# Kernel tuning notes

Hardware: AMD Instinct MI355X
Metric: run time of the kernel (lower is better)

The kernel has to match this reference:

```python
import jax, jax.numpy as jnp
import numpy as np
import math

B, S, H, NH, DH, FF = 8, 512, 1024, 16, 64, 4096


def _layer_norm(x, gamma, beta, eps=1e-12):
    m = jnp.mean(x, axis=-1, keepdims=True)
    v = jnp.mean(jnp.square(x - m), axis=-1, keepdims=True)
    return (x - m) * jax.lax.rsqrt(v + eps) * gamma + beta


def setup_inputs() -> dict:
    key = jax.random.key(0)
    ks = jax.random.split(key, 12)
    w = lambda k, shape: jax.random.normal(k, shape, jnp.float32) * 0.02
    return {
        "layer_input": jax.random.normal(ks[0], (B * S, H), jnp.float32),
        "attention_mask": jax.random.randint(ks[1], (B, S, S), 0, 2, jnp.int32),
        "Wq": w(ks[2], (H, H)), "bq": jnp.zeros((H,), jnp.float32),
        "Wk": w(ks[3], (H, H)), "bk": jnp.zeros((H,), jnp.float32),
        "Wv": w(ks[4], (H, H)), "bv": jnp.zeros((H,), jnp.float32),
        "Wao": w(ks[5], (H, H)), "bao": jnp.zeros((H,), jnp.float32),
        "gamma1": jnp.ones((H,), jnp.float32), "beta1": jnp.zeros((H,), jnp.float32),
        "Wi": w(ks[6], (H, FF)), "bi": jnp.zeros((FF,), jnp.float32),
        "Wo": w(ks[7], (FF, H)), "bo": jnp.zeros((H,), jnp.float32),
        "gamma2": jnp.ones((H,), jnp.float32), "beta2": jnp.zeros((H,), jnp.float32),
        "batch_size": B,
        "seq_length": S,
    }


def reference(layer_input, attention_mask, Wq, bq, Wk, bk, Wv, bv, Wao, bao,
              gamma1, beta1, Wi, bi, Wo, bo, gamma2, beta2, batch_size, seq_length):
    Bs, Sl = batch_size, seq_length
    # QKV projections on flattened [B*S, H]
    q = layer_input @ Wq + bq
    k = layer_input @ Wk + bk
    v = layer_input @ Wv + bv
    # [B*S, H] -> [B, NH, S, DH]
    split = lambda t: t.reshape(Bs, Sl, NH, DH).transpose(0, 2, 1, 3)
    qh, kh, vh = split(q), split(k), split(v)
    # scaled dot-product scores [B, NH, S, S]
    scores = jnp.einsum("bhqd,bhkd->bhqk", qh, kh) * (1.0 / math.sqrt(DH))
    adder = (1.0 - attention_mask[:, None].astype(jnp.float32)) * -10000.0
    probs = jax.nn.softmax(scores + adder, axis=-1)
    # context [B, NH, S, DH] -> [B*S, H]
    ctx = jnp.einsum("bhqk,bhkd->bhqd", probs, vh)
    ctx = ctx.transpose(0, 2, 1, 3).reshape(Bs * Sl, NH * DH)
    attn_out = _layer_norm(ctx @ Wao + bao + layer_input, gamma1, beta1)
    inter = jax.nn.gelu(attn_out @ Wi + bi, approximate=True)  # BERT tanh-gelu
    out = _layer_norm(inter @ Wo + bo + attn_out, gamma2, beta2)
    return out
```

## Files before the change

kernel.cpp:

```cpp
#include <hip/hip_runtime.h>
#include <stdint.h>
#include <math.h>

typedef __attribute__((ext_vector_type(8))) short bf16x8;
typedef __attribute__((ext_vector_type(4))) float f32x4;
typedef __attribute__((ext_vector_type(4))) unsigned short us4;

#define BB   8
#define SS   512
#define HH   1024
#define NHH  16
#define DHH  64
#define FFF  4096
#define MTOK 4096
#define QKVN 3072

__device__ __forceinline__ unsigned short f2bf(float f) {
  union { float f; uint32_t u; } c; c.f = f;
  uint32_t u = c.u;
  return (unsigned short)((u + 0x7fffu + ((u >> 16) & 1u)) >> 16);
}

__device__ __forceinline__ float gelu_tanh(float x) {
  float u = 0.7978845608028654f * (x + 0.044715f * x * x * x);
  return x / (1.0f + __expf(-2.0f * u));
}

__device__ __forceinline__ void gload16(const unsigned short* g, unsigned short* l) {
  __builtin_amdgcn_global_load_lds(
      (const __attribute__((address_space(1))) unsigned short*)g,
      (__attribute__((address_space(3))) unsigned short*)l, 16, 0, 0);
}

__global__ void cast_f32_to_bf16(const float* __restrict__ in,
                                 unsigned short* __restrict__ out, int n4) {
  int i = blockIdx.x * blockDim.x + threadIdx.x;
  if (i >= n4) return;
  f32x4 v = *(const f32x4*)(in + (size_t)i * 4);
  us4 o;
  #pragma unroll
  for (int j = 0; j < 4; ++j) o[j] = f2bf(v[j]);
  *(us4*)(out + (size_t)i * 4) = o;
}

__global__ void transpose_cast(const float* __restrict__ in,
                               unsigned short* __restrict__ out, int R, int C) {
  __shared__ float tile[32][33];
  int bc = blockIdx.x * 32, br = blockIdx.y * 32;
  int tx = threadIdx.x, ty = threadIdx.y;
  #pragma unroll
  for (int i = 0; i < 32; i += 8)
    tile[ty + i][tx] = in[(size_t)(br + ty + i) * C + bc + tx];
  __syncthreads();
  #pragma unroll
  for (int i = 0; i < 32; i += 8)
    out[(size_t)(bc + ty + i) * R + br + tx] = f2bf(tile[tx][ty + i]);
}

__global__ void concat3(const float* __restrict__ a, const float* __restrict__ b,
                        const float* __restrict__ c, float* __restrict__ o) {
  int i = blockIdx.x * 256 + threadIdx.x;
  o[i] = i < HH ? a[i] : (i < 2 * HH ? b[i - HH] : c[i - 2 * HH]);
}

template <int EPI>
__global__ __launch_bounds__(512, 2) void gemm8(
    const unsigned short* __restrict__ A, const unsigned short* __restrict__ BT,
    const float* __restrict__ bias, unsigned short* __restrict__ Cb,
    float* __restrict__ Cf, int M, int N, int K, int KSL) {
  __shared__ unsigned short Asl[2][256 * 64];
  __shared__ unsigned short Bsl[2][256 * 64];
  const int t = threadIdx.x;
  const int w = t >> 6, lane = t & 63;
  const int g = lane >> 4, fr = lane & 15;
  const int wr = w >> 2, wc = w & 3;
  const int m0 = blockIdx.x * 256, n0 = blockIdx.y * 256;
  const int k0 = blockIdx.z * KSL;
  const int nk = KSL >> 6;

  const int srow = t >> 3;
  const int schunk = (t & 7) ^ (srow & 7);
  const unsigned short* gA = A + (size_t)(m0 + srow) * K + k0 + schunk * 8;
  const unsigned short* gB = BT + (size_t)(n0 + srow) * K + k0 + schunk * 8;

  f32x4 acc[8][4] = {};

  #define STAGE(buf, kt)                                                 \
    _Pragma("unroll")                                                    \
    for (int j = 0; j < 4; ++j) {                                        \
      gload16(gA + (size_t)(kt) * 64 + (size_t)j * 64 * K,               \
              &Asl[buf][j * 4096 + w * 512]);                            \
      gload16(gB + (size_t)(kt) * 64 + (size_t)j * 64 * K,               \
              &Bsl[buf][j * 4096 + w * 512]);                            \
    }

  STAGE(0, 0);
  for (int kt = 0; kt < nk; ++kt) {
    const int cur = kt & 1;
    if (kt + 1 < nk) {
      STAGE(cur ^ 1, kt + 1);
      asm volatile("s_waitcnt vmcnt(8)" ::: "memory");
    } else {
      asm volatile("s_waitcnt vmcnt(0)" ::: "memory");
    }
    __builtin_amdgcn_s_barrier();
    bf16x8 bfr[4][2];
    #pragma unroll
    for (int q = 0; q < 4; ++q) {
      if (q == 0) {
        #pragma unroll
        for (int nf = 0; nf < 4; ++nf)
          #pragma unroll
          for (int kk = 0; kk < 2; ++kk)
            bfr[nf][kk] = *(const bf16x8*)(
                &Bsl[cur][(wc * 64 + nf * 16 + fr) * 64 + (((kk * 4 + g) ^ (fr & 7)) * 8)]);
      }
      bf16x8 af[2][2];
      #pragma unroll
      for (int mi = 0; mi < 2; ++mi)
        #pragma unroll
        for (int kk = 0; kk < 2; ++kk)
          af[mi][kk] = *(const bf16x8*)(
              &Asl[cur][(wr * 128 + (q * 2 + mi) * 16 + fr) * 64 + (((kk * 4 + g) ^ (fr & 7)) * 8)]);
      __builtin_amdgcn_s_setprio(1);
      #pragma unroll
      for (int kk = 0; kk < 2; ++kk)
        #pragma unroll
        for (int mi = 0; mi < 2; ++mi)
          #pragma unroll
          for (int nf = 0; nf < 4; ++nf)
            acc[q * 2 + mi][nf] = __builtin_amdgcn_mfma_f32_16x16x32_bf16(
                af[mi][kk], bfr[nf][kk], acc[q * 2 + mi][nf], 0, 0, 0);
      __builtin_amdgcn_s_setprio(0);
      __builtin_amdgcn_s_barrier();
    }
  }
  #undef STAGE

  #pragma unroll
  for (int mf = 0; mf < 8; ++mf) {
    const int gr0 = m0 + wr * 128 + mf * 16 + g * 4;
    #pragma unroll
    for (int nf = 0; nf < 4; ++nf) {
      const int gc = n0 + wc * 64 + nf * 16 + fr;
      const float bb = (EPI == 3) ? 0.f : bias[gc];
      #pragma unroll
      for (int r = 0; r < 4; ++r) {
        float v = acc[mf][nf][r] + bb;
        if (EPI == 2) v = gelu_tanh(v);
        if (EPI == 3)
          Cf[(size_t)blockIdx.z * M * N + (size_t)(gr0 + r) * N + gc] = v;
        else
          Cb[(size_t)(gr0 + r) * N + gc] = f2bf(v);
      }
    }
  }
}

__global__ __launch_bounds__(256) void reduce_split(
    const float* __restrict__ part, const float* __restrict__ bias,
    float* __restrict__ out, int MN, int N, int S) {
  const int i = blockIdx.x * 256 + threadIdx.x;
  f32x4 s = *(const f32x4*)(part + (size_t)i * 4);
  for (int k = 1; k < S; ++k) s += *(const f32x4*)(part + (size_t)k * MN + (size_t)i * 4);
  const int col = (i * 4) & (N - 1);
  f32x4 bv = *(const f32x4*)(bias + col);
  *(f32x4*)(out + (size_t)i * 4) = s + bv;
}

__global__ __launch_bounds__(256) void attn_fused(
    const unsigned short* __restrict__ QKV, const int* __restrict__ mask,
    unsigned short* __restrict__ ctx) {
  __shared__ unsigned short Ks[64][72];
  __shared__ unsigned short Vt[64][72];
  __shared__ unsigned short Pl[4][16][72];
  const int t = threadIdx.x, w = t >> 6, lane = t & 63;
  const int g = lane >> 4, fr = lane & 15;
  const int qt = blockIdx.x;
  const int b = blockIdx.y >> 4, h = blockIdx.y & 15;
  const int colh = h * 64;
  const int qrow0 = b * SS + qt * 64 + w * 16;

  bf16x8 aq[2];
  #pragma unroll
  for (int ks = 0; ks < 2; ++ks)
    aq[ks] = *(const bf16x8*)(QKV + (size_t)(qrow0 + fr) * QKVN + colh + ks * 32 + g * 8);

  float mrow[4], lrow[4];
  f32x4 oacc[4] = {};
  #pragma unroll
  for (int r = 0; r < 4; ++r) { mrow[r] = -INFINITY; lrow[r] = 0.f; }

  for (int kt = 0; kt < 8; ++kt) {
    typedef __attribute__((ext_vector_type(8))) unsigned short us8;
    us8 kr[2], vr[2];
    #pragma unroll
    for (int i = 0; i < 2; ++i) {
      int c = i * 256 + t, row = c >> 3, ko = (c & 7) * 8;
      const size_t gb = (size_t)(b * SS + kt * 64 + row) * QKVN + colh + ko;
      kr[i] = *(const us8*)(QKV + HH + gb);
      vr[i] = *(const us8*)(QKV + 2 * HH + gb);
    }
    __syncthreads();
    #pragma unroll
    for (int i = 0; i < 2; ++i) {
      int c = i * 256 + t, row = c >> 3, ko = (c & 7) * 8;
      *(us8*)(&Ks[row][ko]) = kr[i];
      #pragma unroll
      for (int j = 0; j < 8; ++j) Vt[ko + j][row] = vr[i][j];
    }
    __syncthreads();

    f32x4 sacc[4] = {};
    #pragma unroll
    for (int ks = 0; ks < 2; ++ks)
      #pragma unroll
      for (int cb = 0; cb < 4; ++cb) {
        bf16x8 bk = *(const bf16x8*)(&Ks[cb * 16 + fr][ks * 32 + g * 8]);
        sacc[cb] = __builtin_amdgcn_mfma_f32_16x16x32_bf16(aq[ks], bk, sacc[cb], 0, 0, 0);
      }

    float sv[4][4], nm[4], fac[4], ps[4];
    #pragma unroll
    for (int cb = 0; cb < 4; ++cb) {
      const int kc = kt * 64 + cb * 16 + fr;
      #pragma unroll
      for (int r = 0; r < 4; ++r) {
        const int qg = qt * 64 + w * 16 + g * 4 + r;
        float add = (float)(1 - mask[((size_t)b * SS + qg) * SS + kc]) * -10000.0f;
        sv[cb][r] = sacc[cb][r] * 0.125f + add;
      }
    }
    #pragma unroll
    for (int r = 0; r < 4; ++r)
      nm[r] = fmaxf(fmaxf(sv[0][r], sv[1][r]), fmaxf(sv[2][r], sv[3][r]));
    #pragma unroll
    for (int off = 1; off < 16; off <<= 1)
      #pragma unroll
      for (int r = 0; r < 4; ++r)
        nm[r] = fmaxf(nm[r], __shfl_xor(nm[r], off, 64));
    #pragma unroll
    for (int r = 0; r < 4; ++r) {
      float mn = fmaxf(mrow[r], nm[r]);
      fac[r] = __expf(mrow[r] - mn);
      mrow[r] = mn;
      ps[r] = 0.f;
      #pragma unroll
      for (int cb = 0; cb < 4; ++cb) {
        float pv = __expf(sv[cb][r] - mn);
        sv[cb][r] = pv;
        ps[r] += pv;
      }
    }
    #pragma unroll
    for (int off = 1; off < 16; off <<= 1)
      #pragma unroll
      for (int r = 0; r < 4; ++r)
        ps[r] += __shfl_xor(ps[r], off, 64);
    #pragma unroll
    for (int r = 0; r < 4; ++r) lrow[r] = lrow[r] * fac[r] + ps[r];
    #pragma unroll
    for (int nb = 0; nb < 4; ++nb)
      #pragma unroll
      for (int r = 0; r < 4; ++r) oacc[nb][r] *= fac[r];

    #pragma unroll
    for (int cb = 0; cb < 4; ++cb)
      #pragma unroll
      for (int r = 0; r < 4; ++r)
        Pl[w][g * 4 + r][cb * 16 + fr] = f2bf(sv[cb][r]);
    asm volatile("s_waitcnt lgkmcnt(0)" ::: "memory");

    #pragma unroll
    for (int ks = 0; ks < 2; ++ks) {
      bf16x8 pa = *(const bf16x8*)(&Pl[w][fr][ks * 32 + g * 8]);
      #pragma unroll
      for (int nb = 0; nb < 4; ++nb) {
        bf16x8 bv = *(const bf16x8*)(&Vt[nb * 16 + fr][ks * 32 + g * 8]);
        oacc[nb] = __builtin_amdgcn_mfma_f32_16x16x32_bf16(pa, bv, oacc[nb], 0, 0, 0);
      }
    }
  }
  #pragma unroll
  for (int nb = 0; nb < 4; ++nb)
    #pragma unroll
    for (int r = 0; r < 4; ++r) {
      float v = oacc[nb][r] / lrow[r];
      ctx[(size_t)(qrow0 + g * 4 + r) * HH + colh + nb * 16 + fr] = f2bf(v);
    }
}

__global__ __launch_bounds__(256) void residual_ln(
    const float* __restrict__ x, const float* __restrict__ res,
    const float* __restrict__ gamma, const float* __restrict__ beta,
    float* __restrict__ outf, unsigned short* __restrict__ outb) {
  __shared__ float red[8];
  const int row = blockIdx.x, t = threadIdx.x, w = t >> 6, lane = t & 63;
  const size_t base = (size_t)row * HH + t * 4;
  f32x4 xv = *(const f32x4*)(x + base);
  f32x4 rv = *(const f32x4*)(res + base);
  f32x4 v = xv + rv;
  float s = v[0] + v[1] + v[2] + v[3];
  #pragma unroll
  for (int off = 32; off; off >>= 1) s += __shfl_xor(s, off, 64);
  if (lane == 0) red[w] = s;
  __syncthreads();
  const float mean = (red[0] + red[1] + red[2] + red[3]) * (1.0f / HH);
  f32x4 d;
  #pragma unroll
  for (int j = 0; j < 4; ++j) d[j] = v[j] - mean;
  float q = d[0] * d[0] + d[1] * d[1] + d[2] * d[2] + d[3] * d[3];
  #pragma unroll
  for (int off = 32; off; off >>= 1) q += __shfl_xor(q, off, 64);
  if (lane == 0) red[4 + w] = q;
  __syncthreads();
  const float var = (red[4] + red[5] + red[6] + red[7]) * (1.0f / HH);
  const float rstd = rsqrtf(var + 1e-12f);
  f32x4 gv = *(const f32x4*)(gamma + t * 4);
  f32x4 bv = *(const f32x4*)(beta + t * 4);
  f32x4 o;
  #pragma unroll
  for (int j = 0; j < 4; ++j) o[j] = d[j] * rstd * gv[j] + bv[j];
  *(f32x4*)(outf + base) = o;
  if (outb) {
    us4 ob;
    #pragma unroll
    for (int j = 0; j < 4; ++j) ob[j] = f2bf(o[j]);
    *(us4*)(outb + base) = ob;
  }
}

extern "C" void kernel_launch(void* const* d_in, const int* in_sizes, int n_in,
                              void* d_out, int out_size, void* d_ws, size_t ws_size,
                              hipStream_t stream) {
  const float* lin  = (const float*)d_in[0];
  const int* amask  = (const int*)d_in[1];
  const float* Wq   = (const float*)d_in[2];  const float* bq  = (const float*)d_in[3];
  const float* Wk   = (const float*)d_in[4];  const float* bk  = (const float*)d_in[5];
  const float* Wv   = (const float*)d_in[6];  const float* bv  = (const float*)d_in[7];
  const float* Wao  = (const float*)d_in[8];  const float* bao = (const float*)d_in[9];
  const float* g1   = (const float*)d_in[10]; const float* be1 = (const float*)d_in[11];
  const float* Wi   = (const float*)d_in[12]; const float* bi  = (const float*)d_in[13];
  const float* Wo   = (const float*)d_in[14]; const float* bo  = (const float*)d_in[15];
  const float* g2   = (const float*)d_in[16]; const float* be2 = (const float*)d_in[17];

  char* p = (char*)d_ws;
  const size_t MB = 1024ull * 1024;
  unsigned short* Xb    = (unsigned short*)(p + 0);
  unsigned short* WqkvT = (unsigned short*)(p + 8 * MB);
  unsigned short* WaoT  = (unsigned short*)(p + 14 * MB);
  unsigned short* WiT   = (unsigned short*)(p + 16 * MB);
  unsigned short* WoT   = (unsigned short*)(p + 24 * MB);
  unsigned short* QKVb  = (unsigned short*)(p + 32 * MB);
  unsigned short* Ctx   = (unsigned short*)(p + 56 * MB);
  float*          Tmp   = (float*)(p + 64 * MB);
  float*          Ao    = (float*)(p + 80 * MB);
  unsigned short* Aob   = (unsigned short*)(p + 96 * MB);
  unsigned short* Inter = (unsigned short*)(p + 104 * MB);
  float*          bqkv  = (float*)(p + 104 * MB);
  const bool big = ws_size >= 201 * MB;
  const int SPL = big ? 4 : 2;
  float* PartAO = big ? (float*)(p + 136 * MB) : (float*)(p + 104 * MB);
  float* PartF2 = big ? (float*)(p + 136 * MB) : (float*)(p + 32 * MB);
  (void)in_sizes; (void)n_in; (void)out_size;

  dim3 tb(32, 8);
  cast_f32_to_bf16<<<(MTOK * HH / 4) / 256, 256, 0, stream>>>(lin, Xb, MTOK * HH / 4);
  transpose_cast<<<dim3(HH / 32, HH / 32), tb, 0, stream>>>(Wq, WqkvT, HH, HH);
  transpose_cast<<<dim3(HH / 32, HH / 32), tb, 0, stream>>>(Wk, WqkvT + HH * HH, HH, HH);
  transpose_cast<<<dim3(HH / 32, HH / 32), tb, 0, stream>>>(Wv, WqkvT + 2 * HH * HH, HH, HH);
  transpose_cast<<<dim3(HH / 32, HH / 32), tb, 0, stream>>>(Wao, WaoT, HH, HH);
  transpose_cast<<<dim3(FFF / 32, HH / 32), tb, 0, stream>>>(Wi, WiT, HH, FFF);
  transpose_cast<<<dim3(HH / 32, FFF / 32), tb, 0, stream>>>(Wo, WoT, FFF, HH);
  concat3<<<QKVN / 256, 256, 0, stream>>>(bq, bk, bv, bqkv);

  gemm8<0><<<dim3(MTOK / 256, QKVN / 256), 512, 0, stream>>>(
      Xb, WqkvT, bqkv, QKVb, nullptr, MTOK, QKVN, HH, HH);

  attn_fused<<<dim3(SS / 64, BB * NHH), 256, 0, stream>>>(QKVb, amask, Ctx);

  gemm8<3><<<dim3(MTOK / 256, HH / 256, SPL), 512, 0, stream>>>(
      Ctx, WaoT, nullptr, nullptr, PartAO, MTOK, HH, HH, HH / SPL);
  reduce_split<<<MTOK * HH / 4 / 256, 256, 0, stream>>>(PartAO, bao, Tmp, MTOK * HH, HH, SPL);
  residual_ln<<<MTOK, 256, 0, stream>>>(Tmp, lin, g1, be1, Ao, Aob);

  gemm8<2><<<dim3(MTOK / 256, FFF / 256), 512, 0, stream>>>(
      Aob, WiT, bi, Inter, nullptr, MTOK, FFF, HH, HH);

  gemm8<3><<<dim3(MTOK / 256, HH / 256, SPL), 512, 0, stream>>>(
      Inter, WoT, nullptr, nullptr, PartF2, MTOK, HH, FFF, FFF / SPL);
  reduce_split<<<MTOK * HH / 4 / 256, 256, 0, stream>>>(PartF2, bo, Tmp, MTOK * HH, HH, SPL);
  residual_ln<<<MTOK, 256, 0, stream>>>(Tmp, Ao, g2, be2, (float*)d_out, nullptr);
}
```

Baseline: 401.3 us.

## Fuse split-K reduction into LayerNorm and precompute bf16 mask adder for attention

The separate reduce_split kernels are folded into the residual LayerNorm kernel, which now sums the split-K partials and bias directly. This removes one full fp32 write and read of the intermediate per projection. The int32 mask is converted once into a bf16 additive tensor that attention loads into shared memory and uses to seed the score accumulator, and the next K/V/adder tile is register-prefetched while the current tile is computed. The V transpose in LDS gets an XOR swizzle to cut bank conflicts, and the block index is remapped so batch varies fastest. These changes add an extra mask conversion pass and more LDS use per attention block.

New measurement: 381.8 us. 4.9% less time.

```diff
diff --git a/kernel.cpp b/kernel.cpp
--- a/kernel.cpp
+++ b/kernel.cpp
@@ -5,6 +5,7 @@
 typedef __attribute__((ext_vector_type(8))) short bf16x8;
 typedef __attribute__((ext_vector_type(4))) float f32x4;
 typedef __attribute__((ext_vector_type(4))) unsigned short us4;
+typedef __attribute__((ext_vector_type(8))) unsigned short us8;
 
 #define BB   8
 #define SS   512
@@ -20,6 +21,9 @@
   uint32_t u = c.u;
   return (unsigned short)((u + 0x7fffu + ((u >> 16) & 1u)) >> 16);
 }
+__device__ __forceinline__ float bf2f(unsigned short u) {
+  union { uint32_t u; float f; } c; c.u = ((uint32_t)u) << 16; return c.f;
+}
 
 __device__ __forceinline__ float gelu_tanh(float x) {
   float u = 0.7978845608028654f * (x + 0.044715f * x * x * x);
@@ -41,6 +45,17 @@
   #pragma unroll
   for (int j = 0; j < 4; ++j) o[j] = f2bf(v[j]);
   *(us4*)(out + (size_t)i * 4) = o;
+}
+
+__global__ void mask_to_adder(const int* __restrict__ mask,
+                              unsigned short* __restrict__ out, int n8) {
+  int i = blockIdx.x * 256 + threadIdx.x;
+  if (i >= n8) return;
+  us8 o;
+  #pragma unroll
+  for (int j = 0; j < 8; ++j)
+    o[j] = f2bf((float)(1 - mask[(size_t)i * 8 + j]) * -10000.0f);
+  *(us8*)(out + (size_t)i * 8) = o;
 }
 
 __global__ void transpose_cast(const float* __restrict__ in,
@@ -157,27 +172,17 @@
   }
 }
 
-__global__ __launch_bounds__(256) void reduce_split(
-    const float* __restrict__ part, const float* __restrict__ bias,
-    float* __restrict__ out, int MN, int N, int S) {
-  const int i = blockIdx.x * 256 + threadIdx.x;
-  f32x4 s = *(const f32x4*)(part + (size_t)i * 4);
-  for (int k = 1; k < S; ++k) s += *(const f32x4*)(part + (size_t)k * MN + (size_t)i * 4);
-  const int col = (i * 4) & (N - 1);
-  f32x4 bv = *(const f32x4*)(bias + col);
-  *(f32x4*)(out + (size_t)i * 4) = s + bv;
-}
-
 __global__ __launch_bounds__(256) void attn_fused(
-    const unsigned short* __restrict__ QKV, const int* __restrict__ mask,
+    const unsigned short* __restrict__ QKV, const unsigned short* __restrict__ adder,
     unsigned short* __restrict__ ctx) {
   __shared__ unsigned short Ks[64][72];
   __shared__ unsigned short Vt[64][72];
+  __shared__ unsigned short Al[64][72];
   __shared__ unsigned short Pl[4][16][72];
   const int t = threadIdx.x, w = t >> 6, lane = t & 63;
   const int g = lane >> 4, fr = lane & 15;
-  const int qt = blockIdx.x;
-  const int b = blockIdx.y >> 4, h = blockIdx.y & 15;
+  const int bid = blockIdx.x;
+  const int b = bid & 7, h = (bid >> 3) & 15, qt = bid >> 7;
   const int colh = h * 64;
   const int qrow0 = b * SS + qt * 64 + w * 16;
 
@@ -191,27 +196,38 @@
   #pragma unroll
   for (int r = 0; r < 4; ++r) { mrow[r] = -INFINITY; lrow[r] = 0.f; }
 
+  us8 kr[2], vr[2], ar[2];
+  #define ALOAD(kt)                                                          \
+    _Pragma("unroll")                                                        \
+    for (int i = 0; i < 2; ++i) {                                            \
+      int c = i * 256 + t, row = c >> 3, ko = (c & 7) * 8;                   \
+      const size_t gb = (size_t)(b * SS + (kt) * 64 + row) * QKVN + colh + ko; \
+      kr[i] = *(const us8*)(QKV + HH + gb);                                  \
+      vr[i] = *(const us8*)(QKV + 2 * HH + gb);                              \
+      ar[i] = *(const us8*)(adder + (size_t)(b * SS + qt * 64 + row) * SS + (kt) * 64 + ko); \
+    }
+
+  ALOAD(0);
   for (int kt = 0; kt < 8; ++kt) {
-    typedef __attribute__((ext_vector_type(8))) unsigned short us8;
-    us8 kr[2], vr[2];
-    #pragma unroll
-    for (int i = 0; i < 2; ++i) {
-      int c = i * 256 + t, row = c >> 3, ko = (c & 7) * 8;
-      const size_t gb = (size_t)(b * SS + kt * 64 + row) * QKVN + colh + ko;
-      kr[i] = *(const us8*)(QKV + HH + gb);
-      vr[i] = *(const us8*)(QKV + 2 * HH + gb);
-    }
     __syncthreads();
     #pragma unroll
     for (int i = 0; i < 2; ++i) {
       int c = i * 256 + t, row = c >> 3, ko = (c & 7) * 8;
       *(us8*)(&Ks[row][ko]) = kr[i];
-      #pragma unroll
-      for (int j = 0; j < 8; ++j) Vt[ko + j][row] = vr[i][j];
+      *(us8*)(&Al[row][ko]) = ar[i];
+      const int xo = (row >> 3) ^ (c & 7);
+      #pragma unroll
+      for (int j = 0; j < 8; ++j) Vt[ko + j][xo * 8 + (row & 7)] = vr[i][j];
     }
     __syncthreads();
-
-    f32x4 sacc[4] = {};
+    if (kt < 7) ALOAD(kt + 1);
+
+    f32x4 sacc[4];
+    #pragma unroll
+    for (int cb = 0; cb < 4; ++cb)
+      #pragma unroll
+      for (int r = 0; r < 4; ++r)
+        sacc[cb][r] = 8.0f * bf2f(Al[w * 16 + g * 4 + r][cb * 16 + fr]);
     #pragma unroll
     for (int ks = 0; ks < 2; ++ks)
       #pragma unroll
@@ -222,15 +238,10 @@
 
     float sv[4][4], nm[4], fac[4], ps[4];
     #pragma unroll
-    for (int cb = 0; cb < 4; ++cb) {
-      const int kc = kt * 64 + cb * 16 + fr;
-      #pragma unroll
-      for (int r = 0; r < 4; ++r) {
-        const int qg = qt * 64 + w * 16 + g * 4 + r;
-        float add = (float)(1 - mask[((size_t)b * SS + qg) * SS + kc]) * -10000.0f;
-        sv[cb][r] = sacc[cb][r] * 0.125f + add;
-      }
-    }
+    for (int cb = 0; cb < 4; ++cb)
+      #pragma unroll
+      for (int r = 0; r < 4; ++r)
+        sv[cb][r] = sacc[cb][r] * 0.125f;
     #pragma unroll
     for (int r = 0; r < 4; ++r)
       nm[r] = fmaxf(fmaxf(sv[0][r], sv[1][r]), fmaxf(sv[2][r], sv[3][r]));
@@ -276,11 +287,14 @@
       bf16x8 pa = *(const bf16x8*)(&Pl[w][fr][ks * 32 + g * 8]);
       #pragma unroll
       for (int nb = 0; nb < 4; ++nb) {
-        bf16x8 bv = *(const bf16x8*)(&Vt[nb * 16 + fr][ks * 32 + g * 8]);
+        const int dd = nb * 16 + fr;
+        const int ch = (ks * 4 + g) ^ ((dd >> 3) & 7);
+        bf16x8 bv = *(const bf16x8*)(&Vt[dd][ch * 8]);
         oacc[nb] = __builtin_amdgcn_mfma_f32_16x16x32_bf16(pa, bv, oacc[nb], 0, 0, 0);
       }
     }
   }
+  #undef ALOAD
   #pragma unroll
   for (int nb = 0; nb < 4; ++nb)
     #pragma unroll
@@ -290,20 +304,21 @@
     }
 }
 
-__global__ __launch_bounds__(256) void residual_ln(
-    const float* __restrict__ x, const float* __restrict__ res,
+__global__ __launch_bounds__(256) void residual_ln_red(
+    const float* __restrict__ part, int MN, int S,
+    const float* __restrict__ bias, const float* __restrict__ res,
     const float* __restrict__ gamma, const float* __restrict__ beta,
     float* __restrict__ outf, unsigned short* __restrict__ outb) {
   __shared__ float red[8];
   const int row = blockIdx.x, t = threadIdx.x, w = t >> 6, lane = t & 63;
   const size_t base = (size_t)row * HH + t * 4;
-  f32x4 xv = *(const f32x4*)(x + base);
-  f32x4 rv = *(const f32x4*)(res + base);
-  f32x4 v = xv + rv;
-  float s = v[0] + v[1] + v[2] + v[3];
-  #pragma unroll
-  for (int off = 32; off; off >>= 1) s += __shfl_xor(s, off, 64);
-  if (lane == 0) red[w] = s;
+  f32x4 v = *(const f32x4*)(res + base);
+  v += *(const f32x4*)(bias + t * 4);
+  for (int s = 0; s < S; ++s) v += *(const f32x4*)(part + (size_t)s * MN + base);
+  float sm = v[0] + v[1] + v[2] + v[3];
+  #pragma unroll
+  for (int off = 32; off; off >>= 1) sm += __shfl_xor(sm, off, 64);
+  if (lane == 0) red[w] = sm;
   __syncthreads();
   const float mean = (red[0] + red[1] + red[2] + red[3]) * (1.0f / HH);
   f32x4 d;
@@ -353,11 +368,11 @@
   unsigned short* WoT   = (unsigned short*)(p + 24 * MB);
   unsigned short* QKVb  = (unsigned short*)(p + 32 * MB);
   unsigned short* Ctx   = (unsigned short*)(p + 56 * MB);
-  float*          Tmp   = (float*)(p + 64 * MB);
   float*          Ao    = (float*)(p + 80 * MB);
   unsigned short* Aob   = (unsigned short*)(p + 96 * MB);
   unsigned short* Inter = (unsigned short*)(p + 104 * MB);
-  float*          bqkv  = (float*)(p + 104 * MB);
+  float*          bqkv  = (float*)(p + 64 * MB);
+  unsigned short* adder = (unsigned short*)(p + 66 * MB);
   const bool big = ws_size >= 201 * MB;
   const int SPL = big ? 4 : 2;
   float* PartAO = big ? (float*)(p + 136 * MB) : (float*)(p + 104 * MB);
@@ -366,6 +381,7 @@
 
   dim3 tb(32, 8);
   cast_f32_to_bf16<<<(MTOK * HH / 4) / 256, 256, 0, stream>>>(lin, Xb, MTOK * HH / 4);
+  mask_to_adder<<<(BB * SS * SS / 8) / 256, 256, 0, stream>>>(amask, adder, BB * SS * SS / 8);
   transpose_cast<<<dim3(HH / 32, HH / 32), tb, 0, stream>>>(Wq, WqkvT, HH, HH);
   transpose_cast<<<dim3(HH / 32, HH / 32), tb, 0, stream>>>(Wk, WqkvT + HH * HH, HH, HH);
   transpose_cast<<<dim3(HH / 32, HH / 32), tb, 0, stream>>>(Wv, WqkvT + 2 * HH * HH, HH, HH);
@@ -377,18 +393,17 @@
   gemm8<0><<<dim3(MTOK / 256, QKVN / 256), 512, 0, stream>>>(
       Xb, WqkvT, bqkv, QKVb, nullptr, MTOK, QKVN, HH, HH);
 
-  attn_fused<<<dim3(SS / 64, BB * NHH), 256, 0, stream>>>(QKVb, amask, Ctx);
+  attn_fused<<<SS / 64 * BB * NHH, 256, 0, stream>>>(QKVb, adder, Ctx);
 
   gemm8<3><<<dim3(MTOK / 256, HH / 256, SPL), 512, 0, stream>>>(
       Ctx, WaoT, nullptr, nullptr, PartAO, MTOK, HH, HH, HH / SPL);
-  reduce_split<<<MTOK * HH / 4 / 256, 256, 0, stream>>>(PartAO, bao, Tmp, MTOK * HH, HH, SPL);
-  residual_ln<<<MTOK, 256, 0, stream>>>(Tmp, lin, g1, be1, Ao, Aob);
+  residual_ln_red<<<MTOK, 256, 0, stream>>>(PartAO, MTOK * HH, SPL, bao, lin, g1, be1, Ao, Aob);
 
   gemm8<2><<<dim3(MTOK / 256, FFF / 256), 512, 0, stream>>>(
       Aob, WiT, bi, Inter, nullptr, MTOK, FFF, HH, HH);
 
   gemm8<3><<<dim3(MTOK / 256, HH / 256, SPL), 512, 0, stream>>>(
       Inter, WoT, nullptr, nullptr, PartF2, MTOK, HH, FFF, FFF / SPL);
-  reduce_split<<<MTOK * HH / 4 / 256, 256, 0, stream>>>(PartF2, bo, Tmp, MTOK * HH, HH, SPL);
-  residual_ln<<<MTOK, 256, 0, stream>>>(Tmp, Ao, g2, be2, (float*)d_out, nullptr);
-}
+  residual_ln_red<<<MTOK, 256, 0, stream>>>(PartF2, MTOK * HH, SPL, bo, Ao, g2, be2,
+                                            (float*)d_out, nullptr);
+}
```
